# Kernel tuning notes

Measured on AMD Instinct MI355X. Metric: run time of the kernel, lower is better.

Reference implementation:

```python
import jax, jax.numpy as jnp
import numpy as np

N_MB = 4  # number of micro-behavior buckets; C = N_MB**2 + 1

def setup_inputs() -> dict:
    key = jax.random.key(0)
    k_q, k_k, k_b, k_w, k_a = jax.random.split(key, 5)
    b, h, S, d = 8, 8, 512, 64
    C = N_MB * N_MB + 1
    return {
        "query": jax.random.normal(k_q, (b, h, S, d), dtype=jnp.float32),
        "key": jax.random.normal(k_k, (b, h, S, d), dtype=jnp.float32),
        "b_seq": jax.random.randint(k_b, (b, S), 0, N_MB + 1, dtype=jnp.int32),
        "W1": jax.random.normal(k_w, (N_MB, h, d, d), dtype=jnp.float32) * 0.02,
        "alpha1": jax.random.normal(k_a, (C, N_MB, h), dtype=jnp.float32) * 0.02,
    }

def reference(query, key, b_seq, W1, alpha1):
    # bucket-pair index per (i, j) token pair; 0 if either token is padding
    bi = b_seq[:, :, None]  # [b, S, 1]
    bj = b_seq[:, None, :]  # [b, 1, S]
    b_mat = ((bi - 1) * N_MB + bj) * (bi * bj != 0).astype(jnp.int32)  # [b, S, S]
    # mix the n_mb base bilinear weights into C per-bucket-pair matrices
    W1_ = jnp.einsum('Bhmn,CBh->Chmn', W1, jax.nn.softmax(alpha1, axis=1))
    # full bilinear score for every bucket-pair class C (the wasteful part)
    att_all = jnp.einsum('bhim,Chmn,bhjn->bhijC', query, W1_, key)  # [b,h,S,S,C]
    # select the score matching each pair's bucket index
    idx = b_mat[:, None, :, :, None].astype(jnp.int32)  # [b,1,S,S,1] -> broadcast over h
    idx = jnp.broadcast_to(idx, att_all.shape[:4] + (1,))
    scores = jnp.take_along_axis(att_all, idx, axis=4)[..., 0]  # [b,h,S,S]
    return scores
```

## Files before the change

kernel.cpp:

```cpp
#include <hip/hip_runtime.h>
#include <stdint.h>

#define NB 4
#define NC 17
#define HH 8
#define SS 512
#define DD 64

typedef __attribute__((ext_vector_type(8))) short bf16x8;
typedef __attribute__((ext_vector_type(4))) float f32x4;

#define WS_W1   0
#define WS_RIDX 1114112
#define WS_GST  (WS_RIDX + 16384)

__device__ __forceinline__ unsigned short f2bf(float f) {
  unsigned int x; __builtin_memcpy(&x, &f, 4);
  return (unsigned short)((x + 0x7fff + ((x >> 16) & 1)) >> 16);
}
__device__ __forceinline__ bf16x8 cvt8(const float* p) {
  float4 a = *(const float4*)p;
  float4 b = *(const float4*)(p + 4);
  union { bf16x8 v; unsigned short u[8]; } t;
  t.u[0] = f2bf(a.x); t.u[1] = f2bf(a.y); t.u[2] = f2bf(a.z); t.u[3] = f2bf(a.w);
  t.u[4] = f2bf(b.x); t.u[5] = f2bf(b.y); t.u[6] = f2bf(b.z); t.u[7] = f2bf(b.w);
  return t.v;
}

__global__ __launch_bounds__(256) void k_prep(const int* __restrict__ bseq,
                                              const float* __restrict__ W1,
                                              const float* __restrict__ alpha,
                                              int* __restrict__ ridx,
                                              int* __restrict__ gst,
                                              unsigned short* __restrict__ W1mbf) {
  int tid = threadIdx.x;
  if (blockIdx.x < 8) {
    int b = blockIdx.x;
    __shared__ int cnt[5], base[6], cur[5];
    if (tid < 5) cnt[tid] = 0;
    __syncthreads();
    for (int j = tid; j < SS; j += blockDim.x) atomicAdd(&cnt[bseq[b * SS + j]], 1);
    __syncthreads();
    if (tid == 0) {
      base[0] = 0;
      for (int k = 0; k < 5; k++) base[k + 1] = base[k] + cnt[k];
      for (int k = 0; k < 6; k++) gst[b * 6 + k] = base[k];
    }
    __syncthreads();
    if (tid < 5) cur[tid] = base[tid];
    __syncthreads();
    for (int j = tid; j < SS; j += blockDim.x) {
      int p = atomicAdd(&cur[bseq[b * SS + j]], 1);
      ridx[b * SS + p] = j;
    }
  } else {
    int cb = blockIdx.x - 8;
    int c = cb >> 3, hh = cb & 7;
    __shared__ float sm[NB];
    if (tid == 0) {
      float a[NB], mx = -1e30f;
      for (int B = 0; B < NB; B++) { a[B] = alpha[(c * NB + B) * HH + hh]; mx = fmaxf(mx, a[B]); }
      float s = 0.f;
      for (int B = 0; B < NB; B++) { a[B] = __expf(a[B] - mx); s += a[B]; }
      for (int B = 0; B < NB; B++) sm[B] = a[B] / s;
    }
    __syncthreads();
    float s0 = sm[0], s1 = sm[1], s2 = sm[2], s3 = sm[3];
    for (int idx = tid; idx < DD * DD; idx += blockDim.x) {
      float v = W1[((0 * HH + hh) * DD * DD) + idx] * s0 +
                W1[((1 * HH + hh) * DD * DD) + idx] * s1 +
                W1[((2 * HH + hh) * DD * DD) + idx] * s2 +
                W1[((3 * HH + hh) * DD * DD) + idx] * s3;
      W1mbf[((size_t)(c * HH + hh)) * DD * DD + idx] = f2bf(v);
    }
  }
}

__global__ __launch_bounds__(512) void k_fused(const float* __restrict__ query,
                                               const float* __restrict__ key,
                                               const int* __restrict__ bseq,
                                               const unsigned short* __restrict__ W1mbf,
                                               const int* __restrict__ ridx,
                                               const int* __restrict__ gst,
                                               float* __restrict__ out) {
  int bx = blockIdx.x;
  int jt = bx & 3, bh = bx >> 2, b = bh >> 3, h = bh & 7;
  int j0 = jt * 128;
  int tid = threadIdx.x, wave = tid >> 6, lane = tid & 63;
  int quad = lane >> 4, l16 = lane & 15;

  __shared__ __align__(16) unsigned short Tl[5][128][72];
  __shared__ int ord[128], lgs[6], cnt[5], cur[5];

  if (tid < 5) cnt[tid] = 0;
  __syncthreads();
  int mybj = 0;
  if (tid < 128) { mybj = bseq[b * SS + j0 + tid]; atomicAdd(&cnt[mybj], 1); }
  __syncthreads();
  if (tid == 0) {
    lgs[0] = 0;
    for (int a = 0; a < 5; a++) lgs[a + 1] = lgs[a] + cnt[a];
  }
  __syncthreads();
  if (tid < 5) cur[tid] = lgs[tid];
  __syncthreads();
  if (tid < 128) ord[atomicAdd(&cur[mybj], 1)] = tid;
  __syncthreads();

  int flat = 0;
  for (int a = 0; a < 5; a++) {
    int ls = lgs[a], le = lgs[a + 1];
    if (le <= ls) continue;
    int nB = (a == 0) ? 1 : 5;
    for (int B = 0; B < nB; B++) {
      int c = (B == 0) ? 0 : (B - 1) * NB + a;
      const unsigned short* Wc = W1mbf + (size_t)(c * HH + h) * DD * DD;
      for (int t0 = ls; t0 < le; t0 += 16, flat++) {
        if ((flat & 7) != wave) continue;
        int p = t0 + l16; if (p > le - 1) p = le - 1;
        int cl = ord[p];
        const float* kp = &key[((size_t)(bh * SS + j0 + cl)) * DD + quad * 8];
        bf16x8 af0 = cvt8(kp);
        bf16x8 af1 = cvt8(kp + 32);
        int cr[4];
#pragma unroll
        for (int reg = 0; reg < 4; reg++) {
          int pr = t0 + quad * 4 + reg;
          cr[reg] = (pr < le) ? ord[pr] : -1;
        }
#pragma unroll
        for (int nt = 0; nt < 4; nt++) {
          const unsigned short* wp = &Wc[(nt * 16 + l16) * DD + quad * 8];
          bf16x8 b0 = *(const bf16x8*)wp;
          bf16x8 b1 = *(const bf16x8*)(wp + 32);
          f32x4 acc = {0.f, 0.f, 0.f, 0.f};
          acc = __builtin_amdgcn_mfma_f32_16x16x32_bf16(af0, b0, acc, 0, 0, 0);
          acc = __builtin_amdgcn_mfma_f32_16x16x32_bf16(af1, b1, acc, 0, 0, 0);
#pragma unroll
          for (int reg = 0; reg < 4; reg++) {
            if (cr[reg] >= 0) {
              unsigned short v = f2bf(acc[reg]);
              if (a == 0) {
#pragma unroll
                for (int Bw = 0; Bw < 5; Bw++) Tl[Bw][cr[reg]][nt * 16 + l16] = v;
              } else {
                Tl[B][cr[reg]][nt * 16 + l16] = v;
              }
            }
          }
        }
      }
    }
  }
  __syncthreads();

  flat = 0;
  for (int B = 0; B < 5; B++) {
    int gs = gst[b * 6 + B], ge = gst[b * 6 + B + 1];
    if (ge <= gs) continue;
    for (int p0 = gs; p0 < ge; p0 += 16, flat++) {
      if ((flat & 7) != wave) continue;
      int p = p0 + l16; if (p > ge - 1) p = ge - 1;
      int r = ridx[b * SS + p];
      const float* qp = &query[((size_t)(bh * SS + r)) * DD + quad * 8];
      bf16x8 af0 = cvt8(qp);
      bf16x8 af1 = cvt8(qp + 32);
      int rr[4];
#pragma unroll
      for (int reg = 0; reg < 4; reg++) {
        int pr = p0 + quad * 4 + reg;
        rr[reg] = (pr < ge) ? ridx[b * SS + pr] : -1;
      }
#pragma unroll
      for (int ct = 0; ct < 8; ct++) {
        const unsigned short* tp = &Tl[B][ct * 16 + l16][quad * 8];
        bf16x8 b0 = *(const bf16x8*)tp;
        bf16x8 b1 = *(const bf16x8*)(tp + 32);
        f32x4 acc = {0.f, 0.f, 0.f, 0.f};
        acc = __builtin_amdgcn_mfma_f32_16x16x32_bf16(af0, b0, acc, 0, 0, 0);
        acc = __builtin_amdgcn_mfma_f32_16x16x32_bf16(af1, b1, acc, 0, 0, 0);
#pragma unroll
        for (int reg = 0; reg < 4; reg++)
          if (rr[reg] >= 0)
            out[((size_t)(bh * SS + rr[reg])) * SS + j0 + ct * 16 + l16] = acc[reg];
      }
    }
  }
}

extern "C" void kernel_launch(void* const* d_in, const int* in_sizes, int n_in,
                              void* d_out, int out_size, void* d_ws, size_t ws_size,
                              hipStream_t stream) {
  const float* q = (const float*)d_in[0];
  const float* k = (const float*)d_in[1];
  const int* bseq = (const int*)d_in[2];
  const float* W1 = (const float*)d_in[3];
  const float* alpha = (const float*)d_in[4];
  float* out = (float*)d_out;
  char* ws = (char*)d_ws;
  unsigned short* W1mbf = (unsigned short*)(ws + WS_W1);
  int* ridx = (int*)(ws + WS_RIDX);
  int* gst = (int*)(ws + WS_GST);

  hipLaunchKernelGGL(k_prep, dim3(8 + NC * HH), dim3(256), 0, stream,
                     bseq, W1, alpha, ridx, gst, W1mbf);
  hipLaunchKernelGGL(k_fused, dim3(64 * 4), dim3(512), 0, stream,
                     q, k, bseq, W1mbf, ridx, gst, out);
}
```

Before: 124.2 us.

## Shrink column tile to 32 and precompute per-block work lists for waves

Reduces the key-column tile from 128 to 32, which raises the grid from 256 to 1024 blocks of 256 threads and cuts LDS use per block so more blocks can be resident. Work items for both phases are packed into shared-memory lists so the four waves pull tiles round-robin instead of skipping over a flat counter. In exchange, the query tiles and ridx loads are repeated for every column tile (four times as many query reads), and each output write covers only 32 columns, which shortens the contiguous stores.

After: 138.7 us. 1.12x slower.

```diff
diff --git a/kernel.cpp b/kernel.cpp
--- a/kernel.cpp
+++ b/kernel.cpp
@@ -6,6 +6,7 @@
 #define HH 8
 #define SS 512
 #define DD 64
+#define CT 32
 
 typedef __attribute__((ext_vector_type(8))) short bf16x8;
 typedef __attribute__((ext_vector_type(4))) float f32x4;
@@ -76,7 +77,7 @@
   }
 }
 
-__global__ __launch_bounds__(512) void k_fused(const float* __restrict__ query,
+__global__ __launch_bounds__(256) void k_fused(const float* __restrict__ query,
                                                const float* __restrict__ key,
                                                const int* __restrict__ bseq,
                                                const unsigned short* __restrict__ W1mbf,
@@ -84,18 +85,22 @@
                                                const int* __restrict__ gst,
                                                float* __restrict__ out) {
   int bx = blockIdx.x;
-  int jt = bx & 3, bh = bx >> 2, b = bh >> 3, h = bh & 7;
-  int j0 = jt * 128;
+  int bh = bx & 63, jt = bx >> 6;
+  int b = bh >> 3, h = bh & 7;
+  int j0 = jt * CT;
   int tid = threadIdx.x, wave = tid >> 6, lane = tid & 63;
   int quad = lane >> 4, l16 = lane & 15;
 
-  __shared__ __align__(16) unsigned short Tl[5][128][72];
-  __shared__ int ord[128], lgs[6], cnt[5], cur[5];
+  __shared__ __align__(16) unsigned short Tl[5][CT][72];
+  __shared__ int ord[CT], lgs[6], cnt[5], cur[5];
+  __shared__ int p1list[40], p2list[40];
+  __shared__ int n1s[5], n2s[5], n1b[5], n2b[5];
+  __shared__ int n1tot, n2tot;
 
   if (tid < 5) cnt[tid] = 0;
   __syncthreads();
   int mybj = 0;
-  if (tid < 128) { mybj = bseq[b * SS + j0 + tid]; atomicAdd(&cnt[mybj], 1); }
+  if (tid < CT) { mybj = bseq[b * SS + j0 + tid]; atomicAdd(&cnt[mybj], 1); }
   __syncthreads();
   if (tid == 0) {
     lgs[0] = 0;
@@ -104,49 +109,78 @@
   __syncthreads();
   if (tid < 5) cur[tid] = lgs[tid];
   __syncthreads();
-  if (tid < 128) ord[atomicAdd(&cur[mybj], 1)] = tid;
-  __syncthreads();
-
-  int flat = 0;
-  for (int a = 0; a < 5; a++) {
+  if (tid < CT) ord[atomicAdd(&cur[mybj], 1)] = tid;
+  if (tid < 5) {
+    int a = tid;
+    int tiles = (lgs[a + 1] - lgs[a] + 15) >> 4;
+    n1s[a] = tiles * ((a == 0) ? 1 : 5);
+    int gs = gst[b * 6 + a], ge = gst[b * 6 + a + 1];
+    n2s[a] = (ge - gs + 15) >> 4;
+  }
+  __syncthreads();
+  if (tid == 0) {
+    int a0 = 0, a1 = 0;
+    for (int a = 0; a < 5; a++) {
+      n1b[a] = a0; a0 += n1s[a];
+      n2b[a] = a1; a1 += n2s[a];
+    }
+    n1tot = a0; n2tot = a1;
+  }
+  __syncthreads();
+  if (tid < 5) {
+    int a = tid;
     int ls = lgs[a], le = lgs[a + 1];
-    if (le <= ls) continue;
-    int nB = (a == 0) ? 1 : 5;
-    for (int B = 0; B < nB; B++) {
-      int c = (B == 0) ? 0 : (B - 1) * NB + a;
-      const unsigned short* Wc = W1mbf + (size_t)(c * HH + h) * DD * DD;
-      for (int t0 = ls; t0 < le; t0 += 16, flat++) {
-        if ((flat & 7) != wave) continue;
-        int p = t0 + l16; if (p > le - 1) p = le - 1;
-        int cl = ord[p];
-        const float* kp = &key[((size_t)(bh * SS + j0 + cl)) * DD + quad * 8];
-        bf16x8 af0 = cvt8(kp);
-        bf16x8 af1 = cvt8(kp + 32);
-        int cr[4];
-#pragma unroll
-        for (int reg = 0; reg < 4; reg++) {
-          int pr = t0 + quad * 4 + reg;
-          cr[reg] = (pr < le) ? ord[pr] : -1;
+    int w = n1b[a];
+    for (int t0 = ls; t0 < le; t0 += 16) {
+      if (a == 0) {
+        p1list[w++] = t0 | (le << 5) | (1 << 19);
+      } else {
+        for (int B = 0; B < 5; B++) {
+          int c = (B == 0) ? 0 : (B - 1) * NB + a;
+          p1list[w++] = t0 | (le << 5) | (c << 11) | (B << 16);
         }
-#pragma unroll
-        for (int nt = 0; nt < 4; nt++) {
-          const unsigned short* wp = &Wc[(nt * 16 + l16) * DD + quad * 8];
-          bf16x8 b0 = *(const bf16x8*)wp;
-          bf16x8 b1 = *(const bf16x8*)(wp + 32);
-          f32x4 acc = {0.f, 0.f, 0.f, 0.f};
-          acc = __builtin_amdgcn_mfma_f32_16x16x32_bf16(af0, b0, acc, 0, 0, 0);
-          acc = __builtin_amdgcn_mfma_f32_16x16x32_bf16(af1, b1, acc, 0, 0, 0);
-#pragma unroll
-          for (int reg = 0; reg < 4; reg++) {
-            if (cr[reg] >= 0) {
-              unsigned short v = f2bf(acc[reg]);
-              if (a == 0) {
-#pragma unroll
-                for (int Bw = 0; Bw < 5; Bw++) Tl[Bw][cr[reg]][nt * 16 + l16] = v;
-              } else {
-                Tl[B][cr[reg]][nt * 16 + l16] = v;
-              }
-            }
+      }
+    }
+    int gs = gst[b * 6 + a], ge = gst[b * 6 + a + 1];
+    w = n2b[a];
+    for (int p0 = gs; p0 < ge; p0 += 16)
+      p2list[w++] = p0 | (ge << 10) | (a << 20);
+  }
+  __syncthreads();
+
+  for (int idx = wave; idx < n1tot; idx += 4) {
+    int e = p1list[idx];
+    int t0 = e & 31, le = (e >> 5) & 63, c = (e >> 11) & 31, B = (e >> 16) & 7;
+    int bc = (e >> 19) & 1;
+    const unsigned short* Wc = W1mbf + ((size_t)(c * HH + h) << 12);
+    int p = t0 + l16; if (p > le - 1) p = le - 1;
+    int cl = ord[p];
+    const float* kp = &key[((size_t)(bh * SS + j0 + cl)) * DD + quad * 8];
+    bf16x8 af0 = cvt8(kp);
+    bf16x8 af1 = cvt8(kp + 32);
+    int cr[4];
+#pragma unroll
+    for (int reg = 0; reg < 4; reg++) {
+      int pr = t0 + quad * 4 + reg;
+      cr[reg] = (pr < le) ? ord[pr] : -1;
+    }
+#pragma unroll
+    for (int nt = 0; nt < 4; nt++) {
+      const unsigned short* wp = &Wc[(nt * 16 + l16) * DD + quad * 8];
+      bf16x8 b0 = *(const bf16x8*)wp;
+      bf16x8 b1 = *(const bf16x8*)(wp + 32);
+      f32x4 acc = {0.f, 0.f, 0.f, 0.f};
+      acc = __builtin_amdgcn_mfma_f32_16x16x32_bf16(af0, b0, acc, 0, 0, 0);
+      acc = __builtin_amdgcn_mfma_f32_16x16x32_bf16(af1, b1, acc, 0, 0, 0);
+#pragma unroll
+      for (int reg = 0; reg < 4; reg++) {
+        if (cr[reg] >= 0) {
+          unsigned short v = f2bf(acc[reg]);
+          if (bc) {
+#pragma unroll
+            for (int Bw = 0; Bw < 5; Bw++) Tl[Bw][cr[reg]][nt * 16 + l16] = v;
+          } else {
+            Tl[B][cr[reg]][nt * 16 + l16] = v;
           }
         }
       }
@@ -154,36 +188,32 @@
   }
   __syncthreads();
 
-  flat = 0;
-  for (int B = 0; B < 5; B++) {
-    int gs = gst[b * 6 + B], ge = gst[b * 6 + B + 1];
-    if (ge <= gs) continue;
-    for (int p0 = gs; p0 < ge; p0 += 16, flat++) {
-      if ((flat & 7) != wave) continue;
-      int p = p0 + l16; if (p > ge - 1) p = ge - 1;
-      int r = ridx[b * SS + p];
-      const float* qp = &query[((size_t)(bh * SS + r)) * DD + quad * 8];
-      bf16x8 af0 = cvt8(qp);
-      bf16x8 af1 = cvt8(qp + 32);
-      int rr[4];
-#pragma unroll
-      for (int reg = 0; reg < 4; reg++) {
-        int pr = p0 + quad * 4 + reg;
-        rr[reg] = (pr < ge) ? ridx[b * SS + pr] : -1;
-      }
-#pragma unroll
-      for (int ct = 0; ct < 8; ct++) {
-        const unsigned short* tp = &Tl[B][ct * 16 + l16][quad * 8];
-        bf16x8 b0 = *(const bf16x8*)tp;
-        bf16x8 b1 = *(const bf16x8*)(tp + 32);
-        f32x4 acc = {0.f, 0.f, 0.f, 0.f};
-        acc = __builtin_amdgcn_mfma_f32_16x16x32_bf16(af0, b0, acc, 0, 0, 0);
-        acc = __builtin_amdgcn_mfma_f32_16x16x32_bf16(af1, b1, acc, 0, 0, 0);
-#pragma unroll
-        for (int reg = 0; reg < 4; reg++)
-          if (rr[reg] >= 0)
-            out[((size_t)(bh * SS + rr[reg])) * SS + j0 + ct * 16 + l16] = acc[reg];
-      }
+  for (int idx = wave; idx < n2tot; idx += 4) {
+    int e = p2list[idx];
+    int p0 = e & 1023, ge = (e >> 10) & 1023, B = e >> 20;
+    int p = p0 + l16; if (p > ge - 1) p = ge - 1;
+    int r = ridx[b * SS + p];
+    const float* qp = &query[((size_t)(bh * SS + r)) * DD + quad * 8];
+    bf16x8 af0 = cvt8(qp);
+    bf16x8 af1 = cvt8(qp + 32);
+    int rr[4];
+#pragma unroll
+    for (int reg = 0; reg < 4; reg++) {
+      int pr = p0 + quad * 4 + reg;
+      rr[reg] = (pr < ge) ? ridx[b * SS + pr] : -1;
+    }
+#pragma unroll
+    for (int ct = 0; ct < 2; ct++) {
+      const unsigned short* tp = &Tl[B][ct * 16 + l16][quad * 8];
+      bf16x8 b0 = *(const bf16x8*)tp;
+      bf16x8 b1 = *(const bf16x8*)(tp + 32);
+      f32x4 acc = {0.f, 0.f, 0.f, 0.f};
+      acc = __builtin_amdgcn_mfma_f32_16x16x32_bf16(af0, b0, acc, 0, 0, 0);
+      acc = __builtin_amdgcn_mfma_f32_16x16x32_bf16(af1, b1, acc, 0, 0, 0);
+#pragma unroll
+      for (int reg = 0; reg < 4; reg++)
+        if (rr[reg] >= 0)
+          out[((size_t)(bh * SS + rr[reg])) * SS + j0 + ct * 16 + l16] = acc[reg];
     }
   }
 }
@@ -204,6 +234,6 @@
 
   hipLaunchKernelGGL(k_prep, dim3(8 + NC * HH), dim3(256), 0, stream,
                      bseq, W1, alpha, ridx, gst, W1mbf);
-  hipLaunchKernelGGL(k_fused, dim3(64 * 4), dim3(512), 0, stream,
+  hipLaunchKernelGGL(k_fused, dim3(64 * (SS / CT)), dim3(256), 0, stream,
                      q, k, bseq, W1mbf, ridx, gst, out);
 }
```

## Split fused kernel grid by row-bucket and wider column tiles

Applied to the files above, without the earlier changes.

Restructures the work decomposition so each block handles one (batch,head), one row bucket B, and a 256-column half, instead of all five buckets for a 128-column quarter. Each block now computes only the single T tile needed for its bucket, which shrinks shared memory and lets more blocks run concurrently (640 blocks of 256 threads instead of 256 blocks of 512). In exchange, key-side projection work and the per-block sort of column tokens are repeated once per bucket, and blocks for empty buckets exit early.

After: 128.3 us. 3.3% more time.

```diff
diff --git a/kernel.cpp b/kernel.cpp
--- a/kernel.cpp
+++ b/kernel.cpp
@@ -6,6 +6,7 @@
 #define HH 8
 #define SS 512
 #define DD 64
+#define CT 256
 
 typedef __attribute__((ext_vector_type(8))) short bf16x8;
 typedef __attribute__((ext_vector_type(4))) float f32x4;
@@ -76,7 +77,7 @@
   }
 }
 
-__global__ __launch_bounds__(512) void k_fused(const float* __restrict__ query,
+__global__ __launch_bounds__(256) void k_fused(const float* __restrict__ query,
                                                const float* __restrict__ key,
                                                const int* __restrict__ bseq,
                                                const unsigned short* __restrict__ W1mbf,
@@ -84,18 +85,24 @@
                                                const int* __restrict__ gst,
                                                float* __restrict__ out) {
   int bx = blockIdx.x;
-  int jt = bx & 3, bh = bx >> 2, b = bh >> 3, h = bh & 7;
-  int j0 = jt * 128;
+  int bh = bx & 63, u = bx >> 6;
+  int B = u % 5, half = u / 5;
+  int b = bh >> 3, h = bh & 7;
+  int j0 = half * CT;
   int tid = threadIdx.x, wave = tid >> 6, lane = tid & 63;
   int quad = lane >> 4, l16 = lane & 15;
 
-  __shared__ __align__(16) unsigned short Tl[5][128][72];
-  __shared__ int ord[128], lgs[6], cnt[5], cur[5];
+  int gs = gst[b * 6 + B], ge = gst[b * 6 + B + 1];
+  if (ge <= gs) return;
+
+  __shared__ __align__(16) unsigned short Tl[CT][72];
+  __shared__ int ord[CT], lgs[6], cnt[5], cur[5];
+  __shared__ int p1list[24], n1s[5], n1b[5], n1tot;
 
   if (tid < 5) cnt[tid] = 0;
   __syncthreads();
-  int mybj = 0;
-  if (tid < 128) { mybj = bseq[b * SS + j0 + tid]; atomicAdd(&cnt[mybj], 1); }
+  int mybj = bseq[b * SS + j0 + tid];
+  atomicAdd(&cnt[mybj], 1);
   __syncthreads();
   if (tid == 0) {
     lgs[0] = 0;
@@ -104,86 +111,79 @@
   __syncthreads();
   if (tid < 5) cur[tid] = lgs[tid];
   __syncthreads();
-  if (tid < 128) ord[atomicAdd(&cur[mybj], 1)] = tid;
-  __syncthreads();
-
-  int flat = 0;
-  for (int a = 0; a < 5; a++) {
+  ord[atomicAdd(&cur[mybj], 1)] = tid;
+  if (tid < 5) n1s[tid] = (lgs[tid + 1] - lgs[tid] + 15) >> 4;
+  __syncthreads();
+  if (tid == 0) {
+    int a0 = 0;
+    for (int a = 0; a < 5; a++) { n1b[a] = a0; a0 += n1s[a]; }
+    n1tot = a0;
+  }
+  __syncthreads();
+  if (tid < 5) {
+    int a = tid;
     int ls = lgs[a], le = lgs[a + 1];
-    if (le <= ls) continue;
-    int nB = (a == 0) ? 1 : 5;
-    for (int B = 0; B < nB; B++) {
-      int c = (B == 0) ? 0 : (B - 1) * NB + a;
-      const unsigned short* Wc = W1mbf + (size_t)(c * HH + h) * DD * DD;
-      for (int t0 = ls; t0 < le; t0 += 16, flat++) {
-        if ((flat & 7) != wave) continue;
-        int p = t0 + l16; if (p > le - 1) p = le - 1;
-        int cl = ord[p];
-        const float* kp = &key[((size_t)(bh * SS + j0 + cl)) * DD + quad * 8];
-        bf16x8 af0 = cvt8(kp);
-        bf16x8 af1 = cvt8(kp + 32);
-        int cr[4];
-#pragma unroll
-        for (int reg = 0; reg < 4; reg++) {
-          int pr = t0 + quad * 4 + reg;
-          cr[reg] = (pr < le) ? ord[pr] : -1;
-        }
-#pragma unroll
-        for (int nt = 0; nt < 4; nt++) {
-          const unsigned short* wp = &Wc[(nt * 16 + l16) * DD + quad * 8];
-          bf16x8 b0 = *(const bf16x8*)wp;
-          bf16x8 b1 = *(const bf16x8*)(wp + 32);
-          f32x4 acc = {0.f, 0.f, 0.f, 0.f};
-          acc = __builtin_amdgcn_mfma_f32_16x16x32_bf16(af0, b0, acc, 0, 0, 0);
-          acc = __builtin_amdgcn_mfma_f32_16x16x32_bf16(af1, b1, acc, 0, 0, 0);
-#pragma unroll
-          for (int reg = 0; reg < 4; reg++) {
-            if (cr[reg] >= 0) {
-              unsigned short v = f2bf(acc[reg]);
-              if (a == 0) {
-#pragma unroll
-                for (int Bw = 0; Bw < 5; Bw++) Tl[Bw][cr[reg]][nt * 16 + l16] = v;
-              } else {
-                Tl[B][cr[reg]][nt * 16 + l16] = v;
-              }
-            }
-          }
-        }
-      }
-    }
-  }
-  __syncthreads();
-
-  flat = 0;
-  for (int B = 0; B < 5; B++) {
-    int gs = gst[b * 6 + B], ge = gst[b * 6 + B + 1];
-    if (ge <= gs) continue;
-    for (int p0 = gs; p0 < ge; p0 += 16, flat++) {
-      if ((flat & 7) != wave) continue;
-      int p = p0 + l16; if (p > ge - 1) p = ge - 1;
-      int r = ridx[b * SS + p];
-      const float* qp = &query[((size_t)(bh * SS + r)) * DD + quad * 8];
-      bf16x8 af0 = cvt8(qp);
-      bf16x8 af1 = cvt8(qp + 32);
-      int rr[4];
-#pragma unroll
-      for (int reg = 0; reg < 4; reg++) {
-        int pr = p0 + quad * 4 + reg;
-        rr[reg] = (pr < ge) ? ridx[b * SS + pr] : -1;
-      }
-#pragma unroll
-      for (int ct = 0; ct < 8; ct++) {
-        const unsigned short* tp = &Tl[B][ct * 16 + l16][quad * 8];
-        bf16x8 b0 = *(const bf16x8*)tp;
-        bf16x8 b1 = *(const bf16x8*)(tp + 32);
-        f32x4 acc = {0.f, 0.f, 0.f, 0.f};
-        acc = __builtin_amdgcn_mfma_f32_16x16x32_bf16(af0, b0, acc, 0, 0, 0);
-        acc = __builtin_amdgcn_mfma_f32_16x16x32_bf16(af1, b1, acc, 0, 0, 0);
-#pragma unroll
-        for (int reg = 0; reg < 4; reg++)
-          if (rr[reg] >= 0)
-            out[((size_t)(bh * SS + rr[reg])) * SS + j0 + ct * 16 + l16] = acc[reg];
-      }
+    int c = (B == 0 || a == 0) ? 0 : (B - 1) * NB + a;
+    int w = n1b[a];
+    for (int t0 = ls; t0 < le; t0 += 16)
+      p1list[w++] = t0 | (le << 9) | (c << 18);
+  }
+  __syncthreads();
+
+  for (int idx = wave; idx < n1tot; idx += 4) {
+    int e = p1list[idx];
+    int t0 = e & 511, le = (e >> 9) & 511, c = e >> 18;
+    const unsigned short* Wc = W1mbf + ((size_t)(c * HH + h) << 12);
+    int p = t0 + l16; if (p > le - 1) p = le - 1;
+    int cl = ord[p];
+    const float* kp = &key[((size_t)(bh * SS + j0 + cl)) * DD + quad * 8];
+    bf16x8 af0 = cvt8(kp);
+    bf16x8 af1 = cvt8(kp + 32);
+    int cr[4];
+#pragma unroll
+    for (int reg = 0; reg < 4; reg++) {
+      int pr = t0 + quad * 4 + reg;
+      cr[reg] = (pr < le) ? ord[pr] : -1;
+    }
+#pragma unroll
+    for (int nt = 0; nt < 4; nt++) {
+      const unsigned short* wp = &Wc[(nt * 16 + l16) * DD + quad * 8];
+      bf16x8 b0 = *(const bf16x8*)wp;
+      bf16x8 b1 = *(const bf16x8*)(wp + 32);
+      f32x4 acc = {0.f, 0.f, 0.f, 0.f};
+      acc = __builtin_amdgcn_mfma_f32_16x16x32_bf16(af0, b0, acc, 0, 0, 0);
+      acc = __builtin_amdgcn_mfma_f32_16x16x32_bf16(af1, b1, acc, 0, 0, 0);
+#pragma unroll
+      for (int reg = 0; reg < 4; reg++)
+        if (cr[reg] >= 0) Tl[cr[reg]][nt * 16 + l16] = f2bf(acc[reg]);
+    }
+  }
+  __syncthreads();
+
+  for (int p0 = gs + wave * 16; p0 < ge; p0 += 64) {
+    int p = p0 + l16; if (p > ge - 1) p = ge - 1;
+    int r = ridx[b * SS + p];
+    const float* qp = &query[((size_t)(bh * SS + r)) * DD + quad * 8];
+    bf16x8 af0 = cvt8(qp);
+    bf16x8 af1 = cvt8(qp + 32);
+    int rr[4];
+#pragma unroll
+    for (int reg = 0; reg < 4; reg++) {
+      int pr = p0 + quad * 4 + reg;
+      rr[reg] = (pr < ge) ? ridx[b * SS + pr] : -1;
+    }
+#pragma unroll
+    for (int ct = 0; ct < CT / 16; ct++) {
+      const unsigned short* tp = &Tl[ct * 16 + l16][quad * 8];
+      bf16x8 b0 = *(const bf16x8*)tp;
+      bf16x8 b1 = *(const bf16x8*)(tp + 32);
+      f32x4 acc = {0.f, 0.f, 0.f, 0.f};
+      acc = __builtin_amdgcn_mfma_f32_16x16x32_bf16(af0, b0, acc, 0, 0, 0);
+      acc = __builtin_amdgcn_mfma_f32_16x16x32_bf16(af1, b1, acc, 0, 0, 0);
+#pragma unroll
+      for (int reg = 0; reg < 4; reg++)
+        if (rr[reg] >= 0)
+          out[((size_t)(bh * SS + rr[reg])) * SS + j0 + ct * 16 + l16] = acc[reg];
     }
   }
 }
@@ -204,6 +204,6 @@
 
   hipLaunchKernelGGL(k_prep, dim3(8 + NC * HH), dim3(256), 0, stream,
                      bseq, W1, alpha, ridx, gst, W1mbf);
-  hipLaunchKernelGGL(k_fused, dim3(64 * 4), dim3(512), 0, stream,
+  hipLaunchKernelGGL(k_fused, dim3(64 * 5 * (SS / CT)), dim3(256), 0, stream,
                      q, k, bseq, W1mbf, ridx, gst, out);
 }
```
